# Kernel tuning notes

Hardware: AMD Instinct MI355X
Metric: run time of the kernel (lower is better)

The kernel has to match this reference:

```python
import jax, jax.numpy as jnp
import numpy as np
from jax import lax

DIM = 256
HEADS = 8
SR = 4
EPS = 1e-5
SCALE = (DIM // HEADS) ** -0.5


def _dwconv(x, wgt, stride, pad):
    # x: (B,C,H,W), wgt: (C,1,kh,kw) depthwise
    return lax.conv_general_dilated(
        x, wgt, (stride, stride), [(pad, pad), (pad, pad)],
        feature_group_count=x.shape[1],
        dimension_numbers=("NCHW", "OIHW", "NCHW"))


def _bn(x, g, b, m, v):
    # eval-mode batchnorm folded to per-channel scale/shift
    s = g / jnp.sqrt(v + EPS)
    return x * s[:, None, None] + (b - m * s)[:, None, None]


def setup_inputs() -> dict:
    key = jax.random.key(0)
    ks = jax.random.split(key, 16)
    b, h, w = 8, 64, 64
    c = DIM
    n = h * w

    def rn(k, shape, s=0.05):
        return jax.random.normal(k, shape, jnp.float32) * s

    return dict(
        x=jax.random.normal(ks[0], (b, n, c), jnp.float32),
        h=h, w=w,
        Wq=rn(ks[1], (c, c)), bq=rn(ks[2], (c,)),
        Wkv=rn(ks[3], (2 * c, c)), bkv=rn(ks[4], (2 * c,)),
        sr_w1=rn(ks[5], (c, 1, SR + 3, SR + 3), 0.1),
        bn1_gamma=1.0 + rn(ks[6], (c,)), bn1_beta=rn(ks[7], (c,)),
        bn1_mean=rn(ks[8], (c,)), bn1_var=jnp.abs(1.0 + rn(ks[9], (c,))),
        sr_w2=1.0 + rn(ks[10], (c,), 0.2),  # 1x1 depthwise conv == per-channel scale
        bn2_gamma=1.0 + rn(ks[11], (c,)), bn2_beta=rn(ks[12], (c,)),
        bn2_mean=rn(ks[13], (c,)), bn2_var=jnp.abs(1.0 + rn(ks[14], (c,))),
        local_w=rn(ks[15], (c, 1, 3, 3), 0.1),
        local_b=jnp.zeros((c,), jnp.float32),
    )


def reference(x, h, w, Wq, bq, Wkv, bkv, sr_w1, bn1_gamma, bn1_beta, bn1_mean,
              bn1_var, sr_w2, bn2_gamma, bn2_beta, bn2_mean, bn2_var,
              local_w, local_b):
    b, n, c = x.shape
    hd = c // HEADS
    xi = x.transpose(0, 2, 1).reshape(b, c, h, w)  # (b,c,h,w)

    # q projection (1x1 conv == channel matmul)
    q = jnp.einsum("bchw,dc->bdhw", xi, Wq) + bq[None, :, None, None]
    q = q.reshape(b, HEADS, hd, n).transpose(0, 1, 3, 2)  # (b,H,n,hd)

    # spatial reduction: dwconv7 s4 + BN + GELU + dw1x1 + BN
    kv = _dwconv(xi, sr_w1, SR, (SR + 3) // 2)
    kv = _bn(kv, bn1_gamma, bn1_beta, bn1_mean, bn1_var)
    kv = jax.nn.gelu(kv, approximate=False)
    kv = kv * sr_w2[None, :, None, None]
    kv = _bn(kv, bn2_gamma, bn2_beta, bn2_mean, bn2_var)

    # residual local depthwise 3x3 conv
    kv = _dwconv(kv, local_w, 1, 1) + local_b[None, :, None, None] + kv

    # kv projection and split
    kvp = jnp.einsum("bchw,dc->bdhw", kv, Wkv) + bkv[None, :, None, None]
    k_, v_ = jnp.split(kvp, 2, axis=1)
    m = k_.shape[2] * k_.shape[3]
    k_ = k_.reshape(b, HEADS, hd, m)                       # (b,H,hd,m)
    v_ = v_.reshape(b, HEADS, hd, m).transpose(0, 1, 3, 2)  # (b,H,m,hd)

    attn = jax.nn.softmax(jnp.einsum("bhnd,bhdm->bhnm", q, k_) * SCALE, axis=-1)
    out = jnp.einsum("bhnm,bhmd->bhnd", attn, v_)           # (b,H,n,hd)
    out = out.transpose(0, 1, 3, 2).reshape(b, c, n).transpose(0, 2, 1)
    return out
```

## Files before the change

### kernel.cpp

```cpp
#include <hip/hip_runtime.h>
#include <math.h>

typedef __bf16 bf16;
typedef bf16 bf16x4 __attribute__((ext_vector_type(4)));
typedef bf16 bf16x8 __attribute__((ext_vector_type(8)));
typedef float f32x4 __attribute__((ext_vector_type(4)));

static_assert(sizeof(bf16x8) == 16, "bf16x8 must be 16B");

#define QSCALE (0.17677669529663687f * 1.4426950408889634f)

__device__ __forceinline__ f32x4 mfma16(bf16x8 a, bf16x8 b, f32x4 c) {
  return __builtin_amdgcn_mfma_f32_16x16x32_bf16(a, b, c, 0, 0, 0);
}

__global__ __launch_bounds__(256) void k_cvt(
    const float* __restrict__ Wq, const float* __restrict__ Wkv,
    const float* __restrict__ w7, bf16* __restrict__ Wqb,
    bf16* __restrict__ Wkvb, float* __restrict__ w7t) {
  const int tid = threadIdx.x;
  const int blk = blockIdx.x;
  if (blk < 96) {
    const float* src;
    bf16* dst;
    if (blk < 32) {
      const int idx = blk * 256 + tid;
      src = Wq + (size_t)idx * 8;
      dst = Wqb + (size_t)idx * 8;
    } else {
      const int idx = (blk - 32) * 256 + tid;
      src = Wkv + (size_t)idx * 8;
      dst = Wkvb + (size_t)idx * 8;
    }
    const float4 a = ((const float4*)src)[0];
    const float4 b = ((const float4*)src)[1];
    bf16x8 r;
    r[0] = (bf16)a.x; r[1] = (bf16)a.y; r[2] = (bf16)a.z; r[3] = (bf16)a.w;
    r[4] = (bf16)b.x; r[5] = (bf16)b.y; r[6] = (bf16)b.z; r[7] = (bf16)b.w;
    *(bf16x8*)dst = r;
  } else {
    const int c = tid;
    #pragma unroll
    for (int tap = 0; tap < 49; tap++)
      w7t[tap * 256 + c] = w7[c * 49 + tap];
  }
}

__global__ __launch_bounds__(256) void k_sr(
    const float* __restrict__ x, const float* __restrict__ w7t,
    const float* __restrict__ g1, const float* __restrict__ b1,
    const float* __restrict__ m1, const float* __restrict__ v1,
    const float* __restrict__ sw2,
    const float* __restrict__ g2, const float* __restrict__ b2,
    const float* __restrict__ m2, const float* __restrict__ v2,
    bf16* __restrict__ kv1) {
  __shared__ float part[4][256];
  const int tid = threadIdx.x;
  const int team = tid >> 6, g = tid & 63;
  const int c0 = g * 4;
  const int blk = blockIdx.x;
  const int b = blk & 7, m = blk >> 3;
  const int oy = m >> 4, ox = m & 15;

  float4 xv[13], wv[13];
  float msk[13];
  #pragma unroll
  for (int j = 0; j < 13; j++) {
    const int tap = team + j * 4;
    const int ky = tap / 7, kx = tap - ky * 7;
    const int iy = oy * 4 - 3 + ky, ix = ox * 4 - 3 + kx;
    msk[j] = (tap < 49 && iy >= 0 && iy < 64 && ix >= 0 && ix < 64) ? 1.f : 0.f;
    const int iyc = iy < 0 ? 0 : (iy > 63 ? 63 : iy);
    const int ixc = ix < 0 ? 0 : (ix > 63 ? 63 : ix);
    const int tc = tap > 48 ? 48 : tap;
    xv[j] = *(const float4*)(x + ((size_t)b * 4096 + iyc * 64 + ixc) * 256 + c0);
    wv[j] = *(const float4*)(w7t + tc * 256 + c0);
  }
  float a0 = 0.f, a1 = 0.f, a2 = 0.f, a3 = 0.f;
  #pragma unroll
  for (int j = 0; j < 13; j++) {
    a0 += xv[j].x * wv[j].x * msk[j];
    a1 += xv[j].y * wv[j].y * msk[j];
    a2 += xv[j].z * wv[j].z * msk[j];
    a3 += xv[j].w * wv[j].w * msk[j];
  }
  *(f32x4*)&part[team][c0] = (f32x4){a0, a1, a2, a3};
  __syncthreads();
  const int c = tid;
  float y = part[0][c] + part[1][c] + part[2][c] + part[3][c];
  float s = g1[c] / sqrtf(v1[c] + 1e-5f);
  y = y * s + (b1[c] - m1[c] * s);
  y = 0.5f * y * (1.f + erff(y * 0.70710678118654752f));
  y *= sw2[c];
  s = g2[c] / sqrtf(v2[c] + 1e-5f);
  y = y * s + (b2[c] - m2[c] * s);
  kv1[((size_t)b * 256 + m) * 256 + c] = (bf16)y;
}

__global__ __launch_bounds__(256) void k_localkv(
    const bf16* __restrict__ kv1, const float* __restrict__ w3,
    const float* __restrict__ lb, const bf16* __restrict__ Wkvb,
    const float* __restrict__ bkv, bf16* __restrict__ k_a,
    bf16* __restrict__ v_b) {
  __shared__ bf16 halo[3][10][256];
  __shared__ float rows[8][256];
  const int c = threadIdx.x;
  const int mt = blockIdx.x;
  const int b = blockIdx.y;
  const int oy = mt >> 1, o0 = (mt & 1) * 8;

  #pragma unroll
  for (int p = 0; p < 30; p++) {
    const int dy = p / 10, xi = p - dy * 10;
    const int iy = oy - 1 + dy, ix = o0 - 1 + xi;
    const bool ok = (iy >= 0 && iy < 16 && ix >= 0 && ix < 16);
    const int iyc = ok ? iy : 0, ixc = ok ? ix : 0;
    const bf16 v = kv1[((size_t)b * 256 + iyc * 16 + ixc) * 256 + c];
    halo[dy][xi][c] = ok ? v : (bf16)0.f;
  }
  float w3f[9];
  #pragma unroll
  for (int t = 0; t < 9; t++) w3f[t] = w3[c * 9 + t];
  const float lbf = lb[c];
  __syncthreads();

  #pragma unroll
  for (int r = 0; r < 8; r++) {
    float acc = lbf + (float)halo[1][r + 1][c];
    #pragma unroll
    for (int ky = 0; ky < 3; ky++)
      #pragma unroll
      for (int kx = 0; kx < 3; kx++)
        acc += (float)halo[ky][r + kx][c] * w3f[ky * 3 + kx];
    rows[r][c] = acc;
  }
  __syncthreads();

  const int tid = c;
  float acck[8] = {0}, accv[8] = {0};
  for (int oc = 0; oc < 32; oc++) {
    const bf16x8 w0 = *(const bf16x8*)(Wkvb + (size_t)tid * 256 + oc * 8);
    const bf16x8 w1 = *(const bf16x8*)(Wkvb + ((size_t)tid + 256) * 256 + oc * 8);
    float wf0[8], wf1[8];
    #pragma unroll
    for (int j = 0; j < 8; j++) { wf0[j] = (float)w0[j]; wf1[j] = (float)w1[j]; }
    #pragma unroll
    for (int r = 0; r < 8; r++) {
      const float4* rp = (const float4*)&rows[r][oc * 8];
      const float4 ra = rp[0], rb = rp[1];
      const float rv[8] = {ra.x, ra.y, ra.z, ra.w, rb.x, rb.y, rb.z, rb.w};
      #pragma unroll
      for (int j = 0; j < 8; j++) {
        acck[r] += wf0[j] * rv[j];
        accv[r] += wf1[j] * rv[j];
      }
    }
  }
  const float bk = bkv[tid], bv = bkv[tid + 256];
  const int h = tid >> 5, d = tid & 31;
  #pragma unroll
  for (int r = 0; r < 8; r++) {
    const int m = (oy * 16 + o0) + r;
    k_a[(((size_t)b * 8 + h) * 256 + m) * 32 + d] = (bf16)(acck[r] + bk);
    v_b[(((size_t)b * 8 + h) * 32 + d) * 256 + m] = (bf16)(accv[r] + bv);
  }
}

__global__ __launch_bounds__(256) void k_qproj(
    const float* __restrict__ x, const bf16* __restrict__ Wqb,
    const float* __restrict__ bq, bf16* __restrict__ q_ws) {
  __shared__ bf16 xs[32 * 264];
  const int tid = threadIdx.x, wv = tid >> 6, lane = tid & 63;
  const int qd = lane >> 4, l15 = lane & 15;
  const size_t rowbase = (size_t)blockIdx.x * 32;

  #pragma unroll
  for (int it = 0; it < 4; it++) {
    const int idx = it * 256 + tid;
    const int lr = idx >> 5, pos = idx & 31;
    const float* src = x + (rowbase + lr) * 256 + pos * 8;
    const float4 a = ((const float4*)src)[0];
    const float4 b = ((const float4*)src)[1];
    bf16x8 r;
    r[0] = (bf16)a.x; r[1] = (bf16)a.y; r[2] = (bf16)a.z; r[3] = (bf16)a.w;
    r[4] = (bf16)b.x; r[5] = (bf16)b.y; r[6] = (bf16)b.z; r[7] = (bf16)b.w;
    *(bf16x8*)(xs + lr * 264 + pos * 8) = r;
  }
  __syncthreads();

  f32x4 acc0[4], acc1[4];
  #pragma unroll
  for (int dt = 0; dt < 4; dt++) {
    acc0[dt] = (f32x4){0.f, 0.f, 0.f, 0.f};
    acc1[dt] = (f32x4){0.f, 0.f, 0.f, 0.f};
  }
  #pragma unroll 2
  for (int kc = 0; kc < 8; kc++) {
    const bf16x8 a0 = *(const bf16x8*)(xs + l15 * 264 + kc * 32 + qd * 8);
    const bf16x8 a1 = *(const bf16x8*)(xs + (16 + l15) * 264 + kc * 32 + qd * 8);
    #pragma unroll
    for (int dt = 0; dt < 4; dt++) {
      const int d = wv * 64 + dt * 16 + l15;
      const bf16x8 bb = *(const bf16x8*)(Wqb + (size_t)d * 256 + kc * 32 + qd * 8);
      acc0[dt] = mfma16(a0, bb, acc0[dt]);
      acc1[dt] = mfma16(a1, bb, acc1[dt]);
    }
  }
  #pragma unroll
  for (int dt = 0; dt < 4; dt++) {
    const int d = wv * 64 + dt * 16 + l15;
    const float bias = bq[d];
    const int h = d >> 5, dl = d & 31;
    #pragma unroll
    for (int r = 0; r < 4; r++) {
      const size_t row0 = rowbase + qd * 4 + r;
      const size_t row1 = rowbase + 16 + qd * 4 + r;
      q_ws[(((row0 >> 12) * 8 + h) * 4096 + (row0 & 4095)) * 32 + dl] =
          (bf16)((acc0[dt][r] + bias) * QSCALE);
      q_ws[(((row1 >> 12) * 8 + h) * 4096 + (row1 & 4095)) * 32 + dl] =
          (bf16)((acc1[dt][r] + bias) * QSCALE);
    }
  }
}

__global__ __launch_bounds__(256) void k_attn(
    const bf16* __restrict__ q_ws, const bf16* __restrict__ k_a,
    const bf16* __restrict__ v_b, float* __restrict__ out) {
  const int tid = threadIdx.x;
  const int wv = tid >> 6, lane = tid & 63;
  const int qd = lane >> 4, l15 = lane & 15;
  const int b = blockIdx.z, h = blockIdx.y;
  const int bh = b * 8 + h;
  const int n_base = blockIdx.x * 256 + wv * 64;

  const bf16* qb = q_ws + ((size_t)bh * 4096 + n_base) * 32;
  bf16x8 qf[4];
  #pragma unroll
  for (int qi = 0; qi < 4; qi++)
    qf[qi] = *(const bf16x8*)(qb + (size_t)(qi * 16 + l15) * 32 + qd * 8);

  const bf16* kb = k_a + (size_t)bh * 256 * 32;
  const bf16* vb = v_b + (size_t)bh * 32 * 256;

  f32x4 acc[4][2];
  float lr[4] = {0.f, 0.f, 0.f, 0.f};
  #pragma unroll
  for (int qi = 0; qi < 4; qi++) {
    acc[qi][0] = (f32x4){0.f, 0.f, 0.f, 0.f};
    acc[qi][1] = (f32x4){0.f, 0.f, 0.f, 0.f};
  }
  const int kperm = 8 * (l15 >> 2) + (l15 & 3);

  bf16x8 ka0 = *(const bf16x8*)(kb + (size_t)kperm * 32 + qd * 8);
  bf16x8 ka1 = *(const bf16x8*)(kb + (size_t)(kperm + 4) * 32 + qd * 8);
  bf16x8 va0 = *(const bf16x8*)(vb + (size_t)l15 * 256 + qd * 8);
  bf16x8 va1 = *(const bf16x8*)(vb + (size_t)(16 + l15) * 256 + qd * 8);

  for (int ch = 0; ch < 8; ch++) {
    const int cn = (ch < 7 ? ch + 1 : 7) * 32;
    const bf16x8 nk0 = *(const bf16x8*)(kb + (size_t)(cn + kperm) * 32 + qd * 8);
    const bf16x8 nk1 = *(const bf16x8*)(kb + (size_t)(cn + kperm + 4) * 32 + qd * 8);
    const bf16x8 nv0 = *(const bf16x8*)(vb + (size_t)l15 * 256 + cn + qd * 8);
    const bf16x8 nv1 = *(const bf16x8*)(vb + (size_t)(16 + l15) * 256 + cn + qd * 8);
    const f32x4 z = (f32x4){0.f, 0.f, 0.f, 0.f};
    #pragma unroll
    for (int qi = 0; qi < 4; qi++) {
      f32x4 s0 = mfma16(ka0, qf[qi], z);
      f32x4 s1 = mfma16(ka1, qf[qi], z);
      float p[8], ls = 0.f;
      #pragma unroll
      for (int j = 0; j < 4; j++) {
        p[j] = __builtin_amdgcn_exp2f(fminf(s0[j], 80.f));
        p[4 + j] = __builtin_amdgcn_exp2f(fminf(s1[j], 80.f));
      }
      #pragma unroll
      for (int j = 0; j < 8; j++) ls += p[j];
      lr[qi] += ls;
      bf16x8 pb;
      #pragma unroll
      for (int j = 0; j < 8; j++) pb[j] = (bf16)p[j];
      acc[qi][0] = mfma16(va0, pb, acc[qi][0]);
      acc[qi][1] = mfma16(va1, pb, acc[qi][1]);
    }
    ka0 = nk0; ka1 = nk1; va0 = nv0; va1 = nv1;
  }
  #pragma unroll
  for (int qi = 0; qi < 4; qi++) {
    float l = lr[qi];
    l += __shfl_xor(l, 16, 64);
    l += __shfl_xor(l, 32, 64);
    const float inv = 1.f / l;
    const int nn = n_base + qi * 16 + l15;
    float* ob = out + (size_t)(b * 4096 + nn) * 256 + h * 32;
    #pragma unroll
    for (int t = 0; t < 2; t++) {
      *(float4*)(ob + t * 16 + qd * 4) =
          (float4){acc[qi][t][0] * inv, acc[qi][t][1] * inv,
                   acc[qi][t][2] * inv, acc[qi][t][3] * inv};
    }
  }
}

extern "C" void kernel_launch(void* const* d_in, const int* in_sizes, int n_in,
                              void* d_out, int out_size, void* d_ws, size_t ws_size,
                              hipStream_t stream) {
  const float* x      = (const float*)d_in[0];
  const float* Wq     = (const float*)d_in[3];
  const float* bq     = (const float*)d_in[4];
  const float* Wkv    = (const float*)d_in[5];
  const float* bkv    = (const float*)d_in[6];
  const float* sr_w1  = (const float*)d_in[7];
  const float* bn1_g  = (const float*)d_in[8];
  const float* bn1_b  = (const float*)d_in[9];
  const float* bn1_m  = (const float*)d_in[10];
  const float* bn1_v  = (const float*)d_in[11];
  const float* sw2    = (const float*)d_in[12];
  const float* bn2_g  = (const float*)d_in[13];
  const float* bn2_b  = (const float*)d_in[14];
  const float* bn2_m  = (const float*)d_in[15];
  const float* bn2_v  = (const float*)d_in[16];
  const float* lw     = (const float*)d_in[17];
  const float* lb     = (const float*)d_in[18];

  const int B = in_sizes[0] / (4096 * 256);

  bf16* Wqb  = (bf16*)d_ws;
  bf16* Wkvb = Wqb + 65536;
  float* w7t = (float*)(Wkvb + 131072);
  bf16* kv1  = (bf16*)(w7t + 12544);
  bf16* k_a  = kv1 + (size_t)B * 256 * 256;
  bf16* v_b  = k_a + (size_t)B * 8 * 256 * 32;
  bf16* q_ws = v_b + (size_t)B * 8 * 32 * 256;

  k_cvt<<<dim3(97), 256, 0, stream>>>(Wq, Wkv, sr_w1, Wqb, Wkvb, w7t);
  k_sr<<<dim3(256 * B), 256, 0, stream>>>(x, w7t, bn1_g, bn1_b, bn1_m, bn1_v,
                                          sw2, bn2_g, bn2_b, bn2_m, bn2_v, kv1);
  k_localkv<<<dim3(32, B), 256, 0, stream>>>(kv1, lw, lb, Wkvb, bkv, k_a, v_b);
  k_qproj<<<dim3(B * 128), 256, 0, stream>>>(x, Wqb, bq, q_ws);
  k_attn<<<dim3(16, 8, B), 256, 0, stream>>>(q_ws, k_a, v_b, (float*)d_out);
}
```

Measured before the change: 190.8 us.

## Fuse Q projection into attention kernel, keeping Q in shared memory

Merges the separate Q-projection and attention kernels into one. Each block projects 64 query rows for all 256 channels with MFMA, writes the scaled bf16 Q back into LDS, then loops over the 8 heads to compute softmax-attention against the precomputed K/V. This removes the global Q workspace round trip and one kernel launch. The trade-off is that each wave now handles only 16 queries per head, so K/V fragments are reused less per load. The launch also has fewer blocks and less independent MFMA work per wave, which may hurt latency hiding.

Measured after the change: 229.3 us. +20.2%, slower.

```diff
diff --git a/kernel.cpp b/kernel.cpp
--- a/kernel.cpp
+++ b/kernel.cpp
@@ -166,138 +166,104 @@
   }
 }
 
-__global__ __launch_bounds__(256) void k_qproj(
+__global__ __launch_bounds__(256) void k_qattn(
     const float* __restrict__ x, const bf16* __restrict__ Wqb,
-    const float* __restrict__ bq, bf16* __restrict__ q_ws) {
-  __shared__ bf16 xs[32 * 264];
+    const float* __restrict__ bq, const bf16* __restrict__ k_a,
+    const bf16* __restrict__ v_b, float* __restrict__ out) {
+  __shared__ bf16 qx[64 * 264];
   const int tid = threadIdx.x, wv = tid >> 6, lane = tid & 63;
   const int qd = lane >> 4, l15 = lane & 15;
-  const size_t rowbase = (size_t)blockIdx.x * 32;
-
-  #pragma unroll
-  for (int it = 0; it < 4; it++) {
+  const int b = blockIdx.y;
+  const int n0 = blockIdx.x * 64;
+
+  #pragma unroll
+  for (int it = 0; it < 8; it++) {
     const int idx = it * 256 + tid;
     const int lr = idx >> 5, pos = idx & 31;
-    const float* src = x + (rowbase + lr) * 256 + pos * 8;
+    const float* src = x + ((size_t)b * 4096 + n0 + lr) * 256 + pos * 8;
     const float4 a = ((const float4*)src)[0];
-    const float4 b = ((const float4*)src)[1];
+    const float4 bb = ((const float4*)src)[1];
     bf16x8 r;
-    r[0] = (bf16)a.x; r[1] = (bf16)a.y; r[2] = (bf16)a.z; r[3] = (bf16)a.w;
-    r[4] = (bf16)b.x; r[5] = (bf16)b.y; r[6] = (bf16)b.z; r[7] = (bf16)b.w;
-    *(bf16x8*)(xs + lr * 264 + pos * 8) = r;
+    r[0] = (bf16)a.x;  r[1] = (bf16)a.y;  r[2] = (bf16)a.z;  r[3] = (bf16)a.w;
+    r[4] = (bf16)bb.x; r[5] = (bf16)bb.y; r[6] = (bf16)bb.z; r[7] = (bf16)bb.w;
+    *(bf16x8*)(qx + lr * 264 + pos * 8) = r;
   }
   __syncthreads();
 
-  f32x4 acc0[4], acc1[4];
-  #pragma unroll
-  for (int dt = 0; dt < 4; dt++) {
-    acc0[dt] = (f32x4){0.f, 0.f, 0.f, 0.f};
-    acc1[dt] = (f32x4){0.f, 0.f, 0.f, 0.f};
-  }
-  #pragma unroll 2
-  for (int kc = 0; kc < 8; kc++) {
-    const bf16x8 a0 = *(const bf16x8*)(xs + l15 * 264 + kc * 32 + qd * 8);
-    const bf16x8 a1 = *(const bf16x8*)(xs + (16 + l15) * 264 + kc * 32 + qd * 8);
-    #pragma unroll
-    for (int dt = 0; dt < 4; dt++) {
-      const int d = wv * 64 + dt * 16 + l15;
-      const bf16x8 bb = *(const bf16x8*)(Wqb + (size_t)d * 256 + kc * 32 + qd * 8);
-      acc0[dt] = mfma16(a0, bb, acc0[dt]);
-      acc1[dt] = mfma16(a1, bb, acc1[dt]);
-    }
-  }
-  #pragma unroll
-  for (int dt = 0; dt < 4; dt++) {
-    const int d = wv * 64 + dt * 16 + l15;
+  bf16x8 af[8];
+  #pragma unroll
+  for (int kc = 0; kc < 8; kc++)
+    af[kc] = *(const bf16x8*)(qx + (wv * 16 + l15) * 264 + kc * 32 + qd * 8);
+
+  f32x4 acc[16];
+  #pragma unroll
+  for (int dt = 0; dt < 16; dt++) acc[dt] = (f32x4){0.f, 0.f, 0.f, 0.f};
+  #pragma unroll
+  for (int dt = 0; dt < 16; dt++) {
+    #pragma unroll
+    for (int kc = 0; kc < 8; kc++) {
+      const bf16x8 bb =
+          *(const bf16x8*)(Wqb + (size_t)(dt * 16 + l15) * 256 + kc * 32 + qd * 8);
+      acc[dt] = mfma16(af[kc], bb, acc[dt]);
+    }
+  }
+  #pragma unroll
+  for (int dt = 0; dt < 16; dt++) {
+    const int d = dt * 16 + l15;
     const float bias = bq[d];
-    const int h = d >> 5, dl = d & 31;
     #pragma unroll
     for (int r = 0; r < 4; r++) {
-      const size_t row0 = rowbase + qd * 4 + r;
-      const size_t row1 = rowbase + 16 + qd * 4 + r;
-      q_ws[(((row0 >> 12) * 8 + h) * 4096 + (row0 & 4095)) * 32 + dl] =
-          (bf16)((acc0[dt][r] + bias) * QSCALE);
-      q_ws[(((row1 >> 12) * 8 + h) * 4096 + (row1 & 4095)) * 32 + dl] =
-          (bf16)((acc1[dt][r] + bias) * QSCALE);
-    }
-  }
-}
-
-__global__ __launch_bounds__(256) void k_attn(
-    const bf16* __restrict__ q_ws, const bf16* __restrict__ k_a,
-    const bf16* __restrict__ v_b, float* __restrict__ out) {
-  const int tid = threadIdx.x;
-  const int wv = tid >> 6, lane = tid & 63;
-  const int qd = lane >> 4, l15 = lane & 15;
-  const int b = blockIdx.z, h = blockIdx.y;
-  const int bh = b * 8 + h;
-  const int n_base = blockIdx.x * 256 + wv * 64;
-
-  const bf16* qb = q_ws + ((size_t)bh * 4096 + n_base) * 32;
-  bf16x8 qf[4];
-  #pragma unroll
-  for (int qi = 0; qi < 4; qi++)
-    qf[qi] = *(const bf16x8*)(qb + (size_t)(qi * 16 + l15) * 32 + qd * 8);
-
-  const bf16* kb = k_a + (size_t)bh * 256 * 32;
-  const bf16* vb = v_b + (size_t)bh * 32 * 256;
-
-  f32x4 acc[4][2];
-  float lr[4] = {0.f, 0.f, 0.f, 0.f};
-  #pragma unroll
-  for (int qi = 0; qi < 4; qi++) {
-    acc[qi][0] = (f32x4){0.f, 0.f, 0.f, 0.f};
-    acc[qi][1] = (f32x4){0.f, 0.f, 0.f, 0.f};
-  }
+      const int row = wv * 16 + qd * 4 + r;
+      qx[row * 264 + d] = (bf16)((acc[dt][r] + bias) * QSCALE);
+    }
+  }
+
+  const bf16* kb = k_a + (size_t)(b * 8) * 256 * 32;
+  const bf16* vb = v_b + (size_t)(b * 8) * 32 * 256;
   const int kperm = 8 * (l15 >> 2) + (l15 & 3);
-
-  bf16x8 ka0 = *(const bf16x8*)(kb + (size_t)kperm * 32 + qd * 8);
-  bf16x8 ka1 = *(const bf16x8*)(kb + (size_t)(kperm + 4) * 32 + qd * 8);
-  bf16x8 va0 = *(const bf16x8*)(vb + (size_t)l15 * 256 + qd * 8);
-  bf16x8 va1 = *(const bf16x8*)(vb + (size_t)(16 + l15) * 256 + qd * 8);
-
-  for (int ch = 0; ch < 8; ch++) {
-    const int cn = (ch < 7 ? ch + 1 : 7) * 32;
-    const bf16x8 nk0 = *(const bf16x8*)(kb + (size_t)(cn + kperm) * 32 + qd * 8);
-    const bf16x8 nk1 = *(const bf16x8*)(kb + (size_t)(cn + kperm + 4) * 32 + qd * 8);
-    const bf16x8 nv0 = *(const bf16x8*)(vb + (size_t)l15 * 256 + cn + qd * 8);
-    const bf16x8 nv1 = *(const bf16x8*)(vb + (size_t)(16 + l15) * 256 + cn + qd * 8);
-    const f32x4 z = (f32x4){0.f, 0.f, 0.f, 0.f};
-    #pragma unroll
-    for (int qi = 0; qi < 4; qi++) {
-      f32x4 s0 = mfma16(ka0, qf[qi], z);
-      f32x4 s1 = mfma16(ka1, qf[qi], z);
-      float p[8], ls = 0.f;
+  const int nn = n0 + wv * 16 + l15;
+  float* ob = out + ((size_t)b * 4096 + nn) * 256;
+
+  for (int h = 0; h < 8; h++) {
+    const bf16* kh = kb + (size_t)h * 256 * 32;
+    const bf16* vh = vb + (size_t)h * 32 * 256;
+    const bf16x8 qf =
+        *(const bf16x8*)(qx + (wv * 16 + l15) * 264 + h * 32 + qd * 8);
+    f32x4 a0 = (f32x4){0.f, 0.f, 0.f, 0.f};
+    f32x4 a1 = (f32x4){0.f, 0.f, 0.f, 0.f};
+    float lr = 0.f;
+    #pragma unroll
+    for (int ch = 0; ch < 8; ch++) {
+      const bf16x8 ka0 =
+          *(const bf16x8*)(kh + (size_t)(ch * 32 + kperm) * 32 + qd * 8);
+      const bf16x8 ka1 =
+          *(const bf16x8*)(kh + (size_t)(ch * 32 + kperm + 4) * 32 + qd * 8);
+      const bf16x8 va0 =
+          *(const bf16x8*)(vh + (size_t)l15 * 256 + ch * 32 + qd * 8);
+      const bf16x8 va1 =
+          *(const bf16x8*)(vh + (size_t)(16 + l15) * 256 + ch * 32 + qd * 8);
+      const f32x4 z = (f32x4){0.f, 0.f, 0.f, 0.f};
+      f32x4 s0 = mfma16(ka0, qf, z);
+      f32x4 s1 = mfma16(ka1, qf, z);
+      float p[8];
       #pragma unroll
       for (int j = 0; j < 4; j++) {
         p[j] = __builtin_amdgcn_exp2f(fminf(s0[j], 80.f));
         p[4 + j] = __builtin_amdgcn_exp2f(fminf(s1[j], 80.f));
       }
-      #pragma unroll
-      for (int j = 0; j < 8; j++) ls += p[j];
-      lr[qi] += ls;
       bf16x8 pb;
       #pragma unroll
-      for (int j = 0; j < 8; j++) pb[j] = (bf16)p[j];
-      acc[qi][0] = mfma16(va0, pb, acc[qi][0]);
-      acc[qi][1] = mfma16(va1, pb, acc[qi][1]);
-    }
-    ka0 = nk0; ka1 = nk1; va0 = nv0; va1 = nv1;
-  }
-  #pragma unroll
-  for (int qi = 0; qi < 4; qi++) {
-    float l = lr[qi];
-    l += __shfl_xor(l, 16, 64);
-    l += __shfl_xor(l, 32, 64);
-    const float inv = 1.f / l;
-    const int nn = n_base + qi * 16 + l15;
-    float* ob = out + (size_t)(b * 4096 + nn) * 256 + h * 32;
-    #pragma unroll
-    for (int t = 0; t < 2; t++) {
-      *(float4*)(ob + t * 16 + qd * 4) =
-          (float4){acc[qi][t][0] * inv, acc[qi][t][1] * inv,
-                   acc[qi][t][2] * inv, acc[qi][t][3] * inv};
-    }
+      for (int j = 0; j < 8; j++) { lr += p[j]; pb[j] = (bf16)p[j]; }
+      a0 = mfma16(va0, pb, a0);
+      a1 = mfma16(va1, pb, a1);
+    }
+    lr += __shfl_xor(lr, 16, 64);
+    lr += __shfl_xor(lr, 32, 64);
+    const float inv = 1.f / lr;
+    *(float4*)(ob + h * 32 + qd * 4) =
+        (float4){a0[0] * inv, a0[1] * inv, a0[2] * inv, a0[3] * inv};
+    *(float4*)(ob + h * 32 + 16 + qd * 4) =
+        (float4){a1[0] * inv, a1[1] * inv, a1[2] * inv, a1[3] * inv};
   }
 }
 
@@ -330,12 +296,10 @@
   bf16* kv1  = (bf16*)(w7t + 12544);
   bf16* k_a  = kv1 + (size_t)B * 256 * 256;
   bf16* v_b  = k_a + (size_t)B * 8 * 256 * 32;
-  bf16* q_ws = v_b + (size_t)B * 8 * 32 * 256;
 
   k_cvt<<<dim3(97), 256, 0, stream>>>(Wq, Wkv, sr_w1, Wqb, Wkvb, w7t);
   k_sr<<<dim3(256 * B), 256, 0, stream>>>(x, w7t, bn1_g, bn1_b, bn1_m, bn1_v,
                                           sw2, bn2_g, bn2_b, bn2_m, bn2_v, kv1);
   k_localkv<<<dim3(32, B), 256, 0, stream>>>(kv1, lw, lb, Wkvb, bkv, k_a, v_b);
-  k_qproj<<<dim3(B * 128), 256, 0, stream>>>(x, Wqb, bq, q_ws);
-  k_attn<<<dim3(16, 8, B), 256, 0, stream>>>(q_ws, k_a, v_b, (float*)d_out);
-}
+  k_qattn<<<dim3(64, B), 256, 0, stream>>>(x, Wqb, bq, k_a, v_b, (float*)d_out);
+}
```
